# Performance work log

Measured on AMD Instinct MI355X. Metric: run time of the kernel, lower is better.

Reference implementation:

```python
import jax, jax.numpy as jnp
import numpy as np

N = 4  # hypercomplex dimension

def setup_inputs() -> dict:
    key = jax.random.key(0)
    k1, k2, k3 = jax.random.split(key, 3)
    x = jax.random.normal(k1, (32, 196, 768), dtype=jnp.float32)
    # [n, out_pad/n, in_pad/n] = [4, 3072//4, 768//4]
    weight_components = jax.random.normal(k2, (N, 768, 192), dtype=jnp.float32) * 0.02
    bias = jax.random.normal(k3, (3072,), dtype=jnp.float32) * 0.02
    return {"x": x, "weight_components": weight_components, "bias": bias}

def reference(x, weight_components, bias):
    n, out_blk, in_blk = weight_components.shape
    batch_shape = x.shape[:-1]
    xb = x.reshape(-1, n, in_blk)  # [B, n, in_blk]
    # original: out[:, (i+j)%n] += x[:, j] @ W[i].T
    # equivalently out[:, k] = sum_j x[:, j] @ W[(k-j)%n].T
    k_idx = jnp.arange(n)[:, None]
    j_idx = jnp.arange(n)[None, :]
    Wperm = weight_components[(k_idx - j_idx) % n]  # [n(k), n(j), out_blk, in_blk]
    out = jnp.einsum('bjc,kjoc->bko', xb, Wperm)    # [B, n, out_blk]
    out = out.reshape(-1, n * out_blk) + bias
    return out.reshape(*batch_shape, n * out_blk)
```

## Files before the change

kernel.cpp:

```cpp
#include <hip/hip_runtime.h>
#include <stdint.h>

#define M_ROWS 6272
#define K_DIM  768
#define N_DIM  3072
#define BM 128
#define BN 256
#define BK 32
#define NITER (K_DIM / BK)

#define X_CHUNKS (M_ROWS * K_DIM / 8)
#define W_CHUNKS (N_DIM * K_DIM / 8)
#define X_BLOCKS (X_CHUNKS / 256)
#define W_BLOCKS (W_CHUNKS / 256)

#define GRID_X (N_DIM / BN)
#define GRID_Y (M_ROWS / BM)
#define NWG    (GRID_X * GRID_Y)

typedef unsigned short u16;
typedef __attribute__((ext_vector_type(8))) __bf16 bf16x8;
typedef __attribute__((ext_vector_type(4))) float f32x4;

__device__ __forceinline__ u16 f32_to_bf16(float f) {
    unsigned u = __float_as_uint(f);
    unsigned r = 0x7FFFu + ((u >> 16) & 1u);
    return (u16)((u + r) >> 16);
}

__device__ __forceinline__ unsigned pack2(float a, float b) {
    return (unsigned)f32_to_bf16(a) | ((unsigned)f32_to_bf16(b) << 16);
}

__device__ __forceinline__ void lds_barrier() {
    asm volatile("s_waitcnt lgkmcnt(0)\n\ts_barrier" ::: "memory");
}

#define GLOAD16(gp, lp) __builtin_amdgcn_global_load_lds( \
    (const __attribute__((address_space(1))) void*)(gp),  \
    (__attribute__((address_space(3))) void*)(lp), 16, 0, 0)

__global__ void prep_kernel(const float* __restrict__ x, const float* __restrict__ w,
                            u16* __restrict__ xb, u16* __restrict__ wb) {
    int b = blockIdx.x;
    if (b < X_BLOCKS) {
        int idx = b * 256 + threadIdx.x;
        const float4* xp = (const float4*)x + (size_t)idx * 2;
        float4 a = xp[0], c = xp[1];
        uint4 v;
        v.x = pack2(a.x, a.y);
        v.y = pack2(a.z, a.w);
        v.z = pack2(c.x, c.y);
        v.w = pack2(c.z, c.w);
        ((uint4*)xb)[idx] = v;
    } else {
        int idx = (b - X_BLOCKS) * 256 + threadIdx.x;
        int n    = idx / 96;
        int kc   = idx - n * 96;
        int kblk = n / 768;
        int o    = n - kblk * 768;
        int j    = kc / 24;
        int c8   = kc - j * 24;
        int i    = (kblk - j) & 3;
        const float* src = w + (((size_t)i * 768 + o) * 192 + c8 * 8);
        float4 a = ((const float4*)src)[0];
        float4 c = ((const float4*)src)[1];
        uint4 v;
        v.x = pack2(a.x, a.y);
        v.y = pack2(a.z, a.w);
        v.z = pack2(c.x, c.y);
        v.w = pack2(c.z, c.w);
        ((uint4*)wb)[idx] = v;
    }
}

__global__ __launch_bounds__(512, 4) void gemm_bt(
    const u16* __restrict__ A,
    const u16* __restrict__ B,
    const float* __restrict__ bias,
    float* __restrict__ C)
{
    __shared__ __align__(16) u16 As[3][BM * BK];
    __shared__ __align__(16) u16 Bs[3][BN * BK];

    const int orig = blockIdx.x;
    const int xcd  = orig & 7;
    const int pos  = orig >> 3;
    const int q    = NWG >> 3;
    const int r    = NWG & 7;
    const int lin  = (xcd < r ? xcd * (q + 1) : r * (q + 1) + (xcd - r) * q) + pos;
    const int rowBlk = lin / GRID_X;
    const int colBlk = lin - rowBlk * GRID_X;

    const int rowBase = rowBlk * BM;
    const int colBase = colBlk * BN;

    const int tid    = threadIdx.x;
    const int wave   = tid >> 6;
    const int lane   = tid & 63;
    const int lane16 = lane & 15;
    const int quad   = lane >> 4;
    const int wr     = wave >> 2;
    const int wc     = wave & 3;

    const int cA  = tid;
    const int rA  = cA >> 2,  sA  = (cA & 3) ^ ((rA >> 1) & 3);
    const int cB0 = tid;
    const int cB1 = tid + 512;
    const int rB0 = cB0 >> 2, sB0 = (cB0 & 3) ^ ((rB0 >> 1) & 3);
    const int rB1 = cB1 >> 2, sB1 = (cB1 & 3) ^ ((rB1 >> 1) & 3);

    const uint4* Ag  = (const uint4*)(A + (size_t)(rowBase + rA) * K_DIM + sA * 8);
    const uint4* Bg0 = (const uint4*)(B + (size_t)(colBase + rB0) * K_DIM + sB0 * 8);
    const uint4* Bg1 = (const uint4*)(B + (size_t)(colBase + rB1) * K_DIM + sB1 * 8);

    char* AsB = (char*)As + wave * 1024;
    char* BsB = (char*)Bs + wave * 1024;

#define ISSUE(g, b) do {                                     \
        GLOAD16(Ag  + (g) * 4, AsB + (b) * 8192);            \
        GLOAD16(Bg0 + (g) * 4, BsB + (b) * 16384);           \
        GLOAD16(Bg1 + (g) * 4, BsB + (b) * 16384 + 8192);    \
    } while (0)

    const int swz  = (lane16 >> 1) & 3;
    const int slot = (quad ^ swz) * 8;
    int aoff[4], boff[4];
#pragma unroll
    for (int i = 0; i < 4; ++i)
        aoff[i] = (wr * 64 + i * 16 + lane16) * BK + slot;
#pragma unroll
    for (int j = 0; j < 4; ++j)
        boff[j] = (wc * 64 + j * 16 + lane16) * BK + slot;

    f32x4 acc[4][4] = {};

#define DS_READS(cb)                                                        \
    _Pragma("unroll") for (int i = 0; i < 4; ++i)                           \
        af[i] = *(const bf16x8*)&As[cb][aoff[i]];                           \
    _Pragma("unroll") for (int j = 0; j < 4; ++j)                           \
        bfv[j] = *(const bf16x8*)&Bs[cb][boff[j]];

#define MFMA16()                                                            \
    __builtin_amdgcn_s_setprio(1);                                          \
    _Pragma("unroll") for (int i = 0; i < 4; ++i)                           \
    _Pragma("unroll") for (int j = 0; j < 4; ++j)                           \
        acc[i][j] = __builtin_amdgcn_mfma_f32_16x16x32_bf16(                \
            af[i], bfv[j], acc[i][j], 0, 0, 0);                             \
    __builtin_amdgcn_s_setprio(0);

#define ITER_ISSUE(cb, fb, g) {                                             \
        bf16x8 af[4], bfv[4];                                               \
        DS_READS(cb)                                                        \
        ISSUE(g, fb);                                                       \
        asm volatile("s_waitcnt vmcnt(3)" ::: "memory");                    \
        lds_barrier();                                                      \
        MFMA16()                                                            \
    }

#define ITER_DRAIN(cb) {                                                    \
        bf16x8 af[4], bfv[4];                                               \
        DS_READS(cb)                                                        \
        asm volatile("s_waitcnt vmcnt(0)" ::: "memory");                    \
        lds_barrier();                                                      \
        MFMA16()                                                            \
    }

#define ITER_FINAL(cb) {                                                    \
        bf16x8 af[4], bfv[4];                                               \
        DS_READS(cb)                                                        \
        MFMA16()                                                            \
    }

    ISSUE(0, 0);
    ISSUE(1, 1);
    asm volatile("s_waitcnt vmcnt(3)\n\ts_barrier" ::: "memory");

    for (int t = 0; t < 7; ++t) {
        const int g = t * 3;
        ITER_ISSUE(0, 2, g + 2);
        ITER_ISSUE(1, 0, g + 3);
        ITER_ISSUE(2, 1, g + 4);
    }
    ITER_ISSUE(0, 2, 23);
    ITER_DRAIN(1);
    ITER_FINAL(2);

    float bv[4];
#pragma unroll
    for (int j = 0; j < 4; ++j)
        bv[j] = bias[colBase + wc * 64 + j * 16 + lane16];
#pragma unroll
    for (int i = 0; i < 4; ++i) {
        int row0 = rowBase + wr * 64 + i * 16 + quad * 4;
#pragma unroll
        for (int r2 = 0; r2 < 4; ++r2) {
            float* cp = C + (size_t)(row0 + r2) * N_DIM + colBase + wc * 64 + lane16;
#pragma unroll
            for (int j = 0; j < 4; ++j)
                cp[j * 16] = acc[i][j][r2] + bv[j];
        }
    }
#undef ISSUE
#undef DS_READS
#undef MFMA16
#undef ITER_ISSUE
#undef ITER_DRAIN
#undef ITER_FINAL
}

extern "C" void kernel_launch(void* const* d_in, const int* in_sizes, int n_in,
                              void* d_out, int out_size, void* d_ws, size_t ws_size,
                              hipStream_t stream) {
    const float* x    = (const float*)d_in[0];
    const float* w    = (const float*)d_in[1];
    const float* bias = (const float*)d_in[2];
    float* out = (float*)d_out;

    u16* xb = (u16*)d_ws;
    u16* wb = (u16*)((char*)d_ws + (size_t)M_ROWS * K_DIM * 2);

    hipLaunchKernelGGL(prep_kernel, dim3(X_BLOCKS + W_BLOCKS), dim3(256),
                       0, stream, x, w, xb, wb);
    hipLaunchKernelGGL(gemm_bt, dim3(NWG), dim3(512),
                       0, stream, xb, wb, bias, out);
}
```

Before: 136.2 us.

## Split each K-iteration into two phases interleaving LDS reads, global loads and MFMAs

Each K-step is split into two halves. The first half reads the A fragments plus half of the B fragments, issues two of the three async global-to-LDS loads, and runs 8 MFMAs. The second half reads the remaining B fragments, issues the third load, and runs the other 8 MFMAs, with s_barriers around each MFMA cluster. The goal is finer-grained overlap of memory traffic with matrix math, in the style of ping-pong scheduling. The explicit lgkmcnt wait is dropped, so correctness now depends on compiler-inserted waits for the LDS reads, and the extra barriers may add stalls.

```diff
diff --git a/kernel.cpp b/kernel.cpp
--- a/kernel.cpp
+++ b/kernel.cpp
@@ -30,10 +30,6 @@
 
 __device__ __forceinline__ unsigned pack2(float a, float b) {
     return (unsigned)f32_to_bf16(a) | ((unsigned)f32_to_bf16(b) << 16);
-}
-
-__device__ __forceinline__ void lds_barrier() {
-    asm volatile("s_waitcnt lgkmcnt(0)\n\ts_barrier" ::: "memory");
 }
 
 #define GLOAD16(gp, lp) __builtin_amdgcn_global_load_lds( \
@@ -117,12 +113,6 @@
     char* AsB = (char*)As + wave * 1024;
     char* BsB = (char*)Bs + wave * 1024;
 
-#define ISSUE(g, b) do {                                     \
-        GLOAD16(Ag  + (g) * 4, AsB + (b) * 8192);            \
-        GLOAD16(Bg0 + (g) * 4, BsB + (b) * 16384);           \
-        GLOAD16(Bg1 + (g) * 4, BsB + (b) * 16384 + 8192);    \
-    } while (0)
-
     const int swz  = (lane16 >> 1) & 3;
     const int slot = (quad ^ swz) * 8;
     int aoff[4], boff[4];
@@ -135,45 +125,67 @@
 
     f32x4 acc[4][4] = {};
 
-#define DS_READS(cb)                                                        \
-    _Pragma("unroll") for (int i = 0; i < 4; ++i)                           \
-        af[i] = *(const bf16x8*)&As[cb][aoff[i]];                           \
-    _Pragma("unroll") for (int j = 0; j < 4; ++j)                           \
-        bfv[j] = *(const bf16x8*)&Bs[cb][boff[j]];
-
-#define MFMA16()                                                            \
+#define MFMA_HALF(J0)                                                       \
     __builtin_amdgcn_s_setprio(1);                                          \
     _Pragma("unroll") for (int i = 0; i < 4; ++i)                           \
-    _Pragma("unroll") for (int j = 0; j < 4; ++j)                           \
+    _Pragma("unroll") for (int j = (J0); j < (J0) + 2; ++j)                 \
         acc[i][j] = __builtin_amdgcn_mfma_f32_16x16x32_bf16(                \
             af[i], bfv[j], acc[i][j], 0, 0, 0);                             \
     __builtin_amdgcn_s_setprio(0);
 
-#define ITER_ISSUE(cb, fb, g) {                                             \
+#define ITER_ISSUE(rt, wt, g) {                                             \
         bf16x8 af[4], bfv[4];                                               \
-        DS_READS(cb)                                                        \
-        ISSUE(g, fb);                                                       \
+        _Pragma("unroll") for (int i = 0; i < 4; ++i)                       \
+            af[i] = *(const bf16x8*)&As[rt][aoff[i]];                       \
+        _Pragma("unroll") for (int j = 0; j < 2; ++j)                       \
+            bfv[j] = *(const bf16x8*)&Bs[rt][boff[j]];                      \
+        GLOAD16(Ag  + (g) * 4, AsB + (wt) * 8192);                          \
+        GLOAD16(Bg0 + (g) * 4, BsB + (wt) * 16384);                         \
+        asm volatile("s_barrier" ::: "memory");                             \
+        MFMA_HALF(0)                                                        \
+        asm volatile("s_barrier" ::: "memory");                             \
+        _Pragma("unroll") for (int j = 2; j < 4; ++j)                       \
+            bfv[j] = *(const bf16x8*)&Bs[rt][boff[j]];                      \
+        GLOAD16(Bg1 + (g) * 4, BsB + (wt) * 16384 + 8192);                  \
         asm volatile("s_waitcnt vmcnt(3)" ::: "memory");                    \
-        lds_barrier();                                                      \
-        MFMA16()                                                            \
-    }
-
-#define ITER_DRAIN(cb) {                                                    \
+        asm volatile("s_barrier" ::: "memory");                             \
+        MFMA_HALF(2)                                                        \
+        asm volatile("s_barrier" ::: "memory");                             \
+    }
+
+#define ITER_DRAIN(rt) {                                                    \
         bf16x8 af[4], bfv[4];                                               \
-        DS_READS(cb)                                                        \
+        _Pragma("unroll") for (int i = 0; i < 4; ++i)                       \
+            af[i] = *(const bf16x8*)&As[rt][aoff[i]];                       \
+        _Pragma("unroll") for (int j = 0; j < 2; ++j)                       \
+            bfv[j] = *(const bf16x8*)&Bs[rt][boff[j]];                      \
+        asm volatile("s_barrier" ::: "memory");                             \
+        MFMA_HALF(0)                                                        \
+        asm volatile("s_barrier" ::: "memory");                             \
+        _Pragma("unroll") for (int j = 2; j < 4; ++j)                       \
+            bfv[j] = *(const bf16x8*)&Bs[rt][boff[j]];                      \
         asm volatile("s_waitcnt vmcnt(0)" ::: "memory");                    \
-        lds_barrier();                                                      \
-        MFMA16()                                                            \
-    }
-
-#define ITER_FINAL(cb) {                                                    \
+        asm volatile("s_barrier" ::: "memory");                             \
+        MFMA_HALF(2)                                                        \
+        asm volatile("s_barrier" ::: "memory");                             \
+    }
+
+#define ITER_FINAL(rt) {                                                    \
         bf16x8 af[4], bfv[4];                                               \
-        DS_READS(cb)                                                        \
-        MFMA16()                                                            \
-    }
-
-    ISSUE(0, 0);
-    ISSUE(1, 1);
+        _Pragma("unroll") for (int i = 0; i < 4; ++i)                       \
+            af[i] = *(const bf16x8*)&As[rt][aoff[i]];                       \
+        _Pragma("unroll") for (int j = 0; j < 4; ++j)                       \
+            bfv[j] = *(const bf16x8*)&Bs[rt][boff[j]];                      \
+        MFMA_HALF(0)                                                        \
+        MFMA_HALF(2)                                                        \
+    }
+
+    GLOAD16(Ag,      AsB);
+    GLOAD16(Bg0,     BsB);
+    GLOAD16(Bg1,     BsB + 8192);
+    GLOAD16(Ag  + 4, AsB + 8192);
+    GLOAD16(Bg0 + 4, BsB + 16384);
+    GLOAD16(Bg1 + 4, BsB + 16384 + 8192);
     asm volatile("s_waitcnt vmcnt(3)\n\ts_barrier" ::: "memory");
 
     for (int t = 0; t < 7; ++t) {
@@ -201,9 +213,7 @@
                 cp[j * 16] = acc[i][j][r2] + bv[j];
         }
     }
-#undef ISSUE
-#undef DS_READS
-#undef MFMA16
+#undef MFMA_HALF
 #undef ITER_ISSUE
 #undef ITER_DRAIN
 #undef ITER_FINAL
```

Result: no change. 135.9 us (-0.2%).

## Halve GEMM workgroup to 4 waves each computing a 128x64 tile

Applied to the files above, without the earlier changes.

Shrinks the GEMM workgroup from 8 waves to 4. Each wave now covers all 128 rows by 64 columns (8x4 MFMA tiles) instead of 64x64, and each thread issues six async global-to-LDS loads per stage instead of three. This raises per-wave register reuse of the B fragments and cuts barrier participants. In exchange each wave uses more accumulator registers and there are fewer waves to hide latency, which may lower occupancy.

```diff
diff --git a/kernel.cpp b/kernel.cpp
--- a/kernel.cpp
+++ b/kernel.cpp
@@ -30,10 +30,6 @@
 
 __device__ __forceinline__ unsigned pack2(float a, float b) {
     return (unsigned)f32_to_bf16(a) | ((unsigned)f32_to_bf16(b) << 16);
-}
-
-__device__ __forceinline__ void lds_barrier() {
-    asm volatile("s_waitcnt lgkmcnt(0)\n\ts_barrier" ::: "memory");
 }
 
 #define GLOAD16(gp, lp) __builtin_amdgcn_global_load_lds( \
@@ -74,7 +70,7 @@
     }
 }
 
-__global__ __launch_bounds__(512, 4) void gemm_bt(
+__global__ __launch_bounds__(256, 2) void gemm_bt(
     const u16* __restrict__ A,
     const u16* __restrict__ B,
     const float* __restrict__ bias,
@@ -100,81 +96,79 @@
     const int lane   = tid & 63;
     const int lane16 = lane & 15;
     const int quad   = lane >> 4;
-    const int wr     = wave >> 2;
-    const int wc     = wave & 3;
-
-    const int cA  = tid;
-    const int rA  = cA >> 2,  sA  = (cA & 3) ^ ((rA >> 1) & 3);
-    const int cB0 = tid;
-    const int cB1 = tid + 512;
-    const int rB0 = cB0 >> 2, sB0 = (cB0 & 3) ^ ((rB0 >> 1) & 3);
-    const int rB1 = cB1 >> 2, sB1 = (cB1 & 3) ^ ((rB1 >> 1) & 3);
-
-    const uint4* Ag  = (const uint4*)(A + (size_t)(rowBase + rA) * K_DIM + sA * 8);
-    const uint4* Bg0 = (const uint4*)(B + (size_t)(colBase + rB0) * K_DIM + sB0 * 8);
-    const uint4* Bg1 = (const uint4*)(B + (size_t)(colBase + rB1) * K_DIM + sB1 * 8);
+    const int wc     = wave;
+
+    const int rA = tid >> 2;
+    const int sA = (tid & 3) ^ ((rA >> 1) & 3);
+
+    const uint4* Ag = (const uint4*)(A + (size_t)(rowBase + rA) * K_DIM + sA * 8);
+    const uint4* Bg = (const uint4*)(B + (size_t)(colBase + rA) * K_DIM + sA * 8);
+    const int rowStride = 64 * (K_DIM / 8);
 
     char* AsB = (char*)As + wave * 1024;
     char* BsB = (char*)Bs + wave * 1024;
 
-#define ISSUE(g, b) do {                                     \
-        GLOAD16(Ag  + (g) * 4, AsB + (b) * 8192);            \
-        GLOAD16(Bg0 + (g) * 4, BsB + (b) * 16384);           \
-        GLOAD16(Bg1 + (g) * 4, BsB + (b) * 16384 + 8192);    \
+#define ISSUE(g, b) do {                                                    \
+        GLOAD16(Ag + (g) * 4,                 AsB + (b) * 8192);            \
+        GLOAD16(Ag + (g) * 4 + rowStride,     AsB + (b) * 8192 + 4096);     \
+        GLOAD16(Bg + (g) * 4,                 BsB + (b) * 16384);           \
+        GLOAD16(Bg + (g) * 4 + rowStride,     BsB + (b) * 16384 + 4096);    \
+        GLOAD16(Bg + (g) * 4 + 2 * rowStride, BsB + (b) * 16384 + 8192);    \
+        GLOAD16(Bg + (g) * 4 + 3 * rowStride, BsB + (b) * 16384 + 12288);   \
     } while (0)
 
     const int swz  = (lane16 >> 1) & 3;
     const int slot = (quad ^ swz) * 8;
-    int aoff[4], boff[4];
-#pragma unroll
-    for (int i = 0; i < 4; ++i)
-        aoff[i] = (wr * 64 + i * 16 + lane16) * BK + slot;
+    int aoff[8], boff[4];
+#pragma unroll
+    for (int i = 0; i < 8; ++i)
+        aoff[i] = (i * 16 + lane16) * BK + slot;
 #pragma unroll
     for (int j = 0; j < 4; ++j)
         boff[j] = (wc * 64 + j * 16 + lane16) * BK + slot;
 
-    f32x4 acc[4][4] = {};
+    f32x4 acc[8][4] = {};
 
 #define DS_READS(cb)                                                        \
-    _Pragma("unroll") for (int i = 0; i < 4; ++i)                           \
+    _Pragma("unroll") for (int i = 0; i < 8; ++i)                           \
         af[i] = *(const bf16x8*)&As[cb][aoff[i]];                           \
     _Pragma("unroll") for (int j = 0; j < 4; ++j)                           \
         bfv[j] = *(const bf16x8*)&Bs[cb][boff[j]];
 
-#define MFMA16()                                                            \
+#define MFMA32()                                                            \
     __builtin_amdgcn_s_setprio(1);                                          \
-    _Pragma("unroll") for (int i = 0; i < 4; ++i)                           \
+    _Pragma("unroll") for (int i = 0; i < 8; ++i)                           \
     _Pragma("unroll") for (int j = 0; j < 4; ++j)                           \
         acc[i][j] = __builtin_amdgcn_mfma_f32_16x16x32_bf16(                \
             af[i], bfv[j], acc[i][j], 0, 0, 0);                             \
     __builtin_amdgcn_s_setprio(0);
 
 #define ITER_ISSUE(cb, fb, g) {                                             \
-        bf16x8 af[4], bfv[4];                                               \
+        bf16x8 af[8], bfv[4];                                               \
         DS_READS(cb)                                                        \
         ISSUE(g, fb);                                                       \
-        asm volatile("s_waitcnt vmcnt(3)" ::: "memory");                    \
-        lds_barrier();                                                      \
-        MFMA16()                                                            \
+        asm volatile("s_waitcnt vmcnt(6)" ::: "memory");                    \
+        asm volatile("s_waitcnt lgkmcnt(0)\n\ts_barrier" ::: "memory");     \
+        MFMA32()                                                            \
     }
 
 #define ITER_DRAIN(cb) {                                                    \
-        bf16x8 af[4], bfv[4];                                               \
+        bf16x8 af[8], bfv[4];                                               \
         DS_READS(cb)                                                        \
         asm volatile("s_waitcnt vmcnt(0)" ::: "memory");                    \
-        lds_barrier();                                                      \
-        MFMA16()                                                            \
+        asm volatile("s_waitcnt lgkmcnt(0)\n\ts_barrier" ::: "memory");     \
+        MFMA32()                                                            \
     }
 
 #define ITER_FINAL(cb) {                                                    \
-        bf16x8 af[4], bfv[4];                                               \
+        bf16x8 af[8], bfv[4];                                               \
         DS_READS(cb)                                                        \
-        MFMA16()                                                            \
+        MFMA32()                                                            \
     }
 
     ISSUE(0, 0);
     ISSUE(1, 1);
-    asm volatile("s_waitcnt vmcnt(3)\n\ts_barrier" ::: "memory");
+    asm volatile("s_waitcnt vmcnt(6)\n\ts_barrier" ::: "memory");
 
     for (int t = 0; t < 7; ++t) {
         const int g = t * 3;
@@ -191,8 +185,8 @@
     for (int j = 0; j < 4; ++j)
         bv[j] = bias[colBase + wc * 64 + j * 16 + lane16];
 #pragma unroll
-    for (int i = 0; i < 4; ++i) {
-        int row0 = rowBase + wr * 64 + i * 16 + quad * 4;
+    for (int i = 0; i < 8; ++i) {
+        int row0 = rowBase + i * 16 + quad * 4;
 #pragma unroll
         for (int r2 = 0; r2 < 4; ++r2) {
             float* cp = C + (size_t)(row0 + r2) * N_DIM + colBase + wc * 64 + lane16;
@@ -203,7 +197,7 @@
     }
 #undef ISSUE
 #undef DS_READS
-#undef MFMA16
+#undef MFMA32
 #undef ITER_ISSUE
 #undef ITER_DRAIN
 #undef ITER_FINAL
@@ -222,6 +216,6 @@
 
     hipLaunchKernelGGL(prep_kernel, dim3(X_BLOCKS + W_BLOCKS), dim3(256),
                        0, stream, x, w, xb, wb);
-    hipLaunchKernelGGL(gemm_bt, dim3(NWG), dim3(512),
+    hipLaunchKernelGGL(gemm_bt, dim3(NWG), dim3(256),
                        0, stream, xb, wb, bias, out);
 }
```

Result: no change. 136.1 us (-0.1%).
